# Kernel tuning notes

Measured on AMD Instinct MI355X. Metric: run time of the kernel, lower is better.

Reference implementation:

```python
import math
import jax, jax.numpy as jnp
import numpy as np

T = 4096
D_MODEL = 1024
NUM_HEADS = 16
HEAD_DIM = D_MODEL // NUM_HEADS


def setup_inputs() -> dict:
    key = jax.random.key(0)
    k_x, k_wqkv, k_wproj = jax.random.split(key, 3)
    # match eqx.nn.Linear init scale: U(-1/sqrt(in), 1/sqrt(in)); randn*small works too,
    # but keep magnitudes reasonable so softmax isn't saturated.
    s_in = 1.0 / math.sqrt(D_MODEL)
    x = jax.random.normal(k_x, (T, D_MODEL), dtype=jnp.float32)
    W_qkv = jax.random.normal(k_wqkv, (3 * D_MODEL, D_MODEL), dtype=jnp.float32) * s_in
    b_qkv = jnp.zeros((3 * D_MODEL,), dtype=jnp.float32)
    W_proj = jax.random.normal(k_wproj, (D_MODEL, D_MODEL), dtype=jnp.float32) * s_in
    b_proj = jnp.zeros((D_MODEL,), dtype=jnp.float32)
    return {"x": x, "W_qkv": W_qkv, "b_qkv": b_qkv, "W_proj": W_proj, "b_proj": b_proj}


def reference(x, W_qkv, b_qkv, W_proj, b_proj):
    T_, C = x.shape  # (seq, d_model)
    H, hd = NUM_HEADS, HEAD_DIM
    # c_attn: eqx Linear computes W @ x + b per token -> x @ W.T + b
    qkv = x @ W_qkv.T + b_qkv  # (T, 3C)
    q, k, v = jnp.split(qkv, 3, axis=1)
    # (T, C) -> (H, T, hd)
    q = q.reshape(T_, H, hd).swapaxes(0, 1)
    k = k.reshape(T_, H, hd).swapaxes(0, 1)
    v = v.reshape(T_, H, hd).swapaxes(0, 1)
    scores = jnp.einsum("htd,hsd->hts", q, k) / math.sqrt(hd)  # (H, T, T)
    causal = jnp.tril(jnp.ones((T_, T_), dtype=bool))
    scores = jnp.where(causal, scores, -jnp.inf)
    attn = jax.nn.softmax(scores, axis=-1)
    y = jnp.einsum("hts,hsd->htd", attn, v)  # (H, T, hd)
    y = y.swapaxes(0, 1).reshape(T_, C)
    y = y @ W_proj.T + b_proj
    return y
```

## Files before the change

### kernel.cpp

```cpp
#include <hip/hip_runtime.h>
#include <math.h>
#include <string.h>

#define T_SEQ 4096
#define DM 1024
#define NH 16
#define HD 64

typedef short s8v __attribute__((ext_vector_type(8)));
typedef float f4v __attribute__((ext_vector_type(4)));

__device__ inline unsigned short f2bf(float f) {
    unsigned u; memcpy(&u, &f, 4);
    u = u + 0x7fffu + ((u >> 16) & 1u);
    return (unsigned short)(u >> 16);
}

__device__ inline float exp2fn(float x) {
#if __has_builtin(__builtin_amdgcn_exp2f)
    return __builtin_amdgcn_exp2f(x);
#else
    return exp2f(x);
#endif
}

__device__ inline void gld_lds16(const void* g, void* l) {
    __builtin_amdgcn_global_load_lds(
        (const __attribute__((address_space(1))) void*)g,
        (__attribute__((address_space(3))) void*)l, 16, 0, 0);
}

__global__ __launch_bounds__(256)
void cvt_bf16(const float* __restrict__ in, unsigned short* __restrict__ out, int n8) {
    int i = blockIdx.x * 256 + threadIdx.x;
    if (i >= n8) return;
    const float4* p = (const float4*)(in + (size_t)i * 8);
    float4 a = p[0], b = p[1];
    unsigned short o[8] = {f2bf(a.x), f2bf(a.y), f2bf(a.z), f2bf(a.w),
                           f2bf(b.x), f2bf(b.y), f2bf(b.z), f2bf(b.w)};
    uint4 pk; memcpy(&pk, o, 16);
    *(uint4*)(out + (size_t)i * 8) = pk;
}

template<int MODE>
__global__ __launch_bounds__(256)
void gemm_bt_mfma(const unsigned short* __restrict__ A, const unsigned short* __restrict__ B,
                  const float* __restrict__ bias, void* __restrict__ Cout,
                  unsigned short* __restrict__ vT,
                  int M, int N, int K) {
    __shared__ __align__(16) short As[512 * 8];
    __shared__ __align__(16) short Bs[512 * 8];
    const int tid = threadIdx.x;
    const int w = tid >> 6, lane = tid & 63;
    const int wr = w >> 1, wc = w & 1;
    const int m0 = blockIdx.y * 128, n0 = blockIdx.x * 128;

    const unsigned short* src = (w < 2) ? A : B;
    const int rbase = ((w < 2) ? m0 : n0) + (w & 1) * 64;
    const unsigned short* gsrc = src + (size_t)(rbase + (lane & 15)) * K + ((lane >> 4) * 8);
    short* ldst = ((w < 2) ? As : Bs) + ((w & 1) * 4) * 512;

    f4v acc[4][4];
    #pragma unroll
    for (int i = 0; i < 4; ++i)
        #pragma unroll
        for (int j = 0; j < 4; ++j) acc[i][j] = (f4v){0.f, 0.f, 0.f, 0.f};

    for (int k0 = 0; k0 < K; k0 += 32) {
        __syncthreads();
        #pragma unroll
        for (int i = 0; i < 4; ++i)
            gld_lds16(gsrc + (size_t)(i * 16) * K + k0, ldst + i * 512);
        __syncthreads();

        s8v af[4], bf[4];
        #pragma unroll
        for (int i = 0; i < 4; ++i) af[i] = *(const s8v*)&As[((wr * 4 + i) * 64 + lane) * 8];
        #pragma unroll
        for (int j = 0; j < 4; ++j) bf[j] = *(const s8v*)&Bs[((wc * 4 + j) * 64 + lane) * 8];
        #pragma unroll
        for (int i = 0; i < 4; ++i)
            #pragma unroll
            for (int j = 0; j < 4; ++j)
                acc[i][j] = __builtin_amdgcn_mfma_f32_16x16x32_bf16(af[i], bf[j], acc[i][j], 0, 0, 0);
    }

    const int l15 = lane & 15, quad = lane >> 4;
    float bj[4];
    #pragma unroll
    for (int j = 0; j < 4; ++j) bj[j] = bias[n0 + wc * 64 + j * 16 + l15];

    if (MODE == 2 && n0 >= 2 * DM) {
        #pragma unroll
        for (int i = 0; i < 4; ++i) {
            int tb = m0 + wr * 64 + i * 16 + quad * 4;
            #pragma unroll
            for (int j = 0; j < 4; ++j) {
                int dg = n0 - 2 * DM + wc * 64 + j * 16 + l15;
                unsigned short o[4];
                #pragma unroll
                for (int rg = 0; rg < 4; ++rg) o[rg] = f2bf(acc[i][j][rg] + bj[j]);
                unsigned long long pk; memcpy(&pk, o, 8);
                *(unsigned long long*)&vT[(size_t)dg * T_SEQ + tb] = pk;
            }
        }
    } else {
        #pragma unroll
        for (int i = 0; i < 4; ++i) {
            #pragma unroll
            for (int rg = 0; rg < 4; ++rg) {
                int row = m0 + wr * 64 + i * 16 + quad * 4 + rg;
                #pragma unroll
                for (int j = 0; j < 4; ++j) {
                    int col = n0 + wc * 64 + j * 16 + l15;
                    float v = acc[i][j][rg] + bj[j];
                    if (MODE == 0) ((float*)Cout)[(size_t)row * N + col] = v;
                    else           ((unsigned short*)Cout)[(size_t)row * N + col] = f2bf(v);
                }
            }
        }
    }
}

__global__ __launch_bounds__(256, 2)
void attn_mfma2(const unsigned short* __restrict__ qkv,
                const unsigned short* __restrict__ vT,
                unsigned short* __restrict__ y) {
    const int b = blockIdx.x;
    const int h = b & 15, a = b >> 4;
    const int tid = threadIdx.x;
    const int w = tid >> 6, lane = tid & 63;
    const int quad = lane >> 4, l15 = lane & 15;
    const int cq = h * HD, hv = h * HD;
    const size_t rs = 3 * DM;
    const float C2 = 0.1803368851f;

    __shared__ short KB[2][4096];
    __shared__ short VTs[2][4096];
    __shared__ short QB[4096];
    __shared__ short PB[4][1024];

    for (int ph = 0; ph < 2; ++ph) {
        const int qt = ph ? (63 - a) : a;
        const int q0 = qt * 64;

        __syncthreads();
        #pragma unroll
        for (int rr = 0; rr < 2; ++rr) {
            int ch = rr * 256 + tid;
            int blk = ch >> 7, hf = (ch >> 6) & 1, ln = ch & 63;
            const unsigned short* gq = qkv + (size_t)(q0 + blk * 16 + (ln & 15)) * rs
                                     + cq + hf * 32 + ((ln >> 4) << 3);
            gld_lds16(gq, &QB[(ch & ~63) * 8]);
            const unsigned short* gk = qkv + (size_t)(blk * 16 + (ln & 15)) * rs
                                     + DM + cq + hf * 32 + ((ln >> 4) << 3);
            gld_lds16(gk, &KB[0][(ch & ~63) * 8]);
            const unsigned short* gv = vT + (size_t)(hv + blk * 16 + (ln & 15)) * T_SEQ
                                     + hf * 32 + ((ln >> 4) << 3);
            gld_lds16(gv, &VTs[0][(ch & ~63) * 8]);
        }
        __syncthreads();

        s8v qf0 = *(const s8v*)&QB[((w * 2 + 0) * 64 + lane) * 8];
        s8v qf1 = *(const s8v*)&QB[((w * 2 + 1) * 64 + lane) * 8];

        f4v O[4];
        #pragma unroll
        for (int ob = 0; ob < 4; ++ob) O[ob] = (f4v){0.f, 0.f, 0.f, 0.f};
        float mr = -3.0e38f, lr = 0.f;

        for (int kt = 0; kt <= qt; ++kt) {
            const int p = kt & 1;
            if (kt < qt) {
                const int k1 = (kt + 1) * 64;
                #pragma unroll
                for (int rr = 0; rr < 2; ++rr) {
                    int ch = rr * 256 + tid;
                    int blk = ch >> 7, hf = (ch >> 6) & 1, ln = ch & 63;
                    const unsigned short* gk = qkv + (size_t)(k1 + blk * 16 + (ln & 15)) * rs
                                             + DM + cq + hf * 32 + ((ln >> 4) << 3);
                    gld_lds16(gk, &KB[p ^ 1][(ch & ~63) * 8]);
                    const unsigned short* gv = vT + (size_t)(hv + blk * 16 + (ln & 15)) * T_SEQ
                                             + k1 + hf * 32 + ((ln >> 4) << 3);
                    gld_lds16(gv, &VTs[p ^ 1][(ch & ~63) * 8]);
                }
            }

            f4v st[4];
            #pragma unroll
            for (int kb = 0; kb < 4; ++kb) {
                s8v k0f = *(const s8v*)&KB[p][((kb * 2 + 0) * 64 + lane) * 8];
                s8v k1f = *(const s8v*)&KB[p][((kb * 2 + 1) * 64 + lane) * 8];
                f4v c = (f4v){0.f, 0.f, 0.f, 0.f};
                c = __builtin_amdgcn_mfma_f32_16x16x32_bf16(k0f, qf0, c, 0, 0, 0);
                c = __builtin_amdgcn_mfma_f32_16x16x32_bf16(k1f, qf1, c, 0, 0, 0);
                st[kb] = c;
            }

            float sv[4][4];
            #pragma unroll
            for (int kb = 0; kb < 4; ++kb)
                #pragma unroll
                for (int rg = 0; rg < 4; ++rg) sv[kb][rg] = st[kb][rg];
            if (kt == qt) {
                #pragma unroll
                for (int kb = 0; kb < 4; ++kb) {
                    #pragma unroll
                    for (int rg = 0; rg < 4; ++rg)
                        if (kb * 16 + quad * 4 + rg > w * 16 + l15) sv[kb][rg] = -3.0e38f;
                }
            }

            float mx = sv[0][0];
            #pragma unroll
            for (int kb = 0; kb < 4; ++kb)
                #pragma unroll
                for (int rg = 0; rg < 4; ++rg) mx = fmaxf(mx, sv[kb][rg]);
            mx = fmaxf(mx, __shfl_xor(mx, 16));
            mx = fmaxf(mx, __shfl_xor(mx, 32));
            float mn = fmaxf(mr, mx);
            float alpha = exp2fn((mr - mn) * C2);
            float mc = mn * C2;
            float ps = 0.f;
            #pragma unroll
            for (int kb = 0; kb < 4; ++kb)
                #pragma unroll
                for (int rg = 0; rg < 4; ++rg) {
                    float t = exp2fn(fmaf(sv[kb][rg], C2, -mc));
                    sv[kb][rg] = t;
                    ps += t;
                }
            ps += __shfl_xor(ps, 16);
            ps += __shfl_xor(ps, 32);
            lr = lr * alpha + ps;
            mr = mn;
            #pragma unroll
            for (int ob = 0; ob < 4; ++ob)
                #pragma unroll
                for (int rg = 0; rg < 4; ++rg) O[ob][rg] *= alpha;

            short* pw = PB[w];
            #pragma unroll
            for (int kb = 0; kb < 4; ++kb) {
                unsigned u0 = __float_as_uint(sv[kb][0]) + 0x8000u;
                unsigned u1 = __float_as_uint(sv[kb][1]) + 0x8000u;
                unsigned u2 = __float_as_uint(sv[kb][2]) + 0x8000u;
                unsigned u3 = __float_as_uint(sv[kb][3]) + 0x8000u;
                int2 v;
                v.x = (int)__builtin_amdgcn_perm(u1, u0, 0x07060302);
                v.y = (int)__builtin_amdgcn_perm(u3, u2, 0x07060302);
                int c = (kb >> 1) * 64 + ((kb & 1) * 2 + (quad >> 1)) * 16 + l15;
                c ^= ((c >> 3) & 7);
                *(int2*)&pw[c * 8 + (quad & 1) * 4] = v;
            }
            asm volatile("s_waitcnt lgkmcnt(0)" ::: "memory");
            int c0 = lane ^ ((lane >> 3) & 7);
            s8v pf0 = *(const s8v*)&pw[c0 * 8];
            s8v pf1 = *(const s8v*)&pw[(64 + c0) * 8];

            #pragma unroll
            for (int ob = 0; ob < 4; ++ob) {
                s8v v0f = *(const s8v*)&VTs[p][((ob * 2 + 0) * 64 + lane) * 8];
                s8v v1f = *(const s8v*)&VTs[p][((ob * 2 + 1) * 64 + lane) * 8];
                O[ob] = __builtin_amdgcn_mfma_f32_16x16x32_bf16(v0f, pf0, O[ob], 0, 0, 0);
                O[ob] = __builtin_amdgcn_mfma_f32_16x16x32_bf16(v1f, pf1, O[ob], 0, 0, 0);
            }
            __syncthreads();
        }

        float linv = 1.f / lr;
        size_t ybase = (size_t)(q0 + w * 16 + l15) * DM + cq;
        #pragma unroll
        for (int ob = 0; ob < 4; ++ob) {
            unsigned short o[4];
            #pragma unroll
            for (int rg = 0; rg < 4; ++rg) o[rg] = f2bf(O[ob][rg] * linv);
            unsigned long long pk; memcpy(&pk, o, 8);
            *(unsigned long long*)&y[ybase + ob * 16 + quad * 4] = pk;
        }
    }
}

extern "C" void kernel_launch(void* const* d_in, const int* in_sizes, int n_in,
                              void* d_out, int out_size, void* d_ws, size_t ws_size,
                              hipStream_t stream) {
    const float* x     = (const float*)d_in[0];
    const float* Wqkv  = (const float*)d_in[1];
    const float* bqkv  = (const float*)d_in[2];
    const float* Wproj = (const float*)d_in[3];
    const float* bproj = (const float*)d_in[4];
    float* out = (float*)d_out;

    char* ws = (char*)d_ws;
    unsigned short* qkvb  = (unsigned short*)(ws);
    unsigned short* yattb = (unsigned short*)(ws + (24u << 20));
    unsigned short* xb    = (unsigned short*)(ws + (32u << 20));
    unsigned short* wqkvb = (unsigned short*)(ws + (40u << 20));
    unsigned short* wprjb = (unsigned short*)(ws + (46u << 20));
    unsigned short* vTb   = (unsigned short*)(ws + (48u << 20));

    dim3 blk(256);
    {
        int n8;
        n8 = T_SEQ * DM / 8;
        cvt_bf16<<<dim3((n8 + 255) / 256), blk, 0, stream>>>(x, xb, n8);
        n8 = 3 * DM * DM / 8;
        cvt_bf16<<<dim3((n8 + 255) / 256), blk, 0, stream>>>(Wqkv, wqkvb, n8);
        n8 = DM * DM / 8;
        cvt_bf16<<<dim3((n8 + 255) / 256), blk, 0, stream>>>(Wproj, wprjb, n8);
    }
    gemm_bt_mfma<2><<<dim3(3 * DM / 128, T_SEQ / 128), blk, 0, stream>>>(
        xb, wqkvb, bqkv, qkvb, vTb, T_SEQ, 3 * DM, DM);
    attn_mfma2<<<dim3(NH * 32), blk, 0, stream>>>(qkvb, vTb, yattb);
    gemm_bt_mfma<0><<<dim3(DM / 128, T_SEQ / 128), blk, 0, stream>>>(
        yattb, wprjb, bproj, out, nullptr, T_SEQ, DM, DM);
}
```

Before: 242.2 us.

## Use 128-row query tiles in attention, fuse conversions, narrow proj GEMM tile

The attention kernel now gives each block one 128-row query tile split into two 64-row groups that share every staged K/V tile. This halves K/V loads per query and removes the two-phase loop. The three fp32-to-bf16 conversions become a single launch, cutting launch overhead. The output projection GEMM uses a 64-wide N tile so it launches more blocks, at the cost of less reuse per block and idle staging warps.

```diff
diff --git a/kernel.cpp b/kernel.cpp
--- a/kernel.cpp
+++ b/kernel.cpp
@@ -31,72 +31,83 @@
 }
 
 __global__ __launch_bounds__(256)
-void cvt_bf16(const float* __restrict__ in, unsigned short* __restrict__ out, int n8) {
+void cvt3(const float* __restrict__ i0, unsigned short* __restrict__ o0, int n0,
+          const float* __restrict__ i1, unsigned short* __restrict__ o1, int n1,
+          const float* __restrict__ i2, unsigned short* __restrict__ o2, int n2) {
     int i = blockIdx.x * 256 + threadIdx.x;
-    if (i >= n8) return;
-    const float4* p = (const float4*)(in + (size_t)i * 8);
+    const float* in; unsigned short* out; int j;
+    if (i < n0)           { in = i0; out = o0; j = i; }
+    else if (i < n0 + n1) { in = i1; out = o1; j = i - n0; }
+    else if (i < n0 + n1 + n2) { in = i2; out = o2; j = i - n0 - n1; }
+    else return;
+    const float4* p = (const float4*)(in + (size_t)j * 8);
     float4 a = p[0], b = p[1];
     unsigned short o[8] = {f2bf(a.x), f2bf(a.y), f2bf(a.z), f2bf(a.w),
                            f2bf(b.x), f2bf(b.y), f2bf(b.z), f2bf(b.w)};
     uint4 pk; memcpy(&pk, o, 16);
-    *(uint4*)(out + (size_t)i * 8) = pk;
-}
-
-template<int MODE>
+    *(uint4*)(out + (size_t)j * 8) = pk;
+}
+
+template<int MODE, int TN>
 __global__ __launch_bounds__(256)
 void gemm_bt_mfma(const unsigned short* __restrict__ A, const unsigned short* __restrict__ B,
                   const float* __restrict__ bias, void* __restrict__ Cout,
                   unsigned short* __restrict__ vT,
                   int M, int N, int K) {
-    __shared__ __align__(16) short As[512 * 8];
-    __shared__ __align__(16) short Bs[512 * 8];
+    constexpr int NF = TN / 32;
+    __shared__ __align__(16) short As[4096];
+    __shared__ __align__(16) short Bs[TN * 32];
     const int tid = threadIdx.x;
     const int w = tid >> 6, lane = tid & 63;
     const int wr = w >> 1, wc = w & 1;
-    const int m0 = blockIdx.y * 128, n0 = blockIdx.x * 128;
-
-    const unsigned short* src = (w < 2) ? A : B;
-    const int rbase = ((w < 2) ? m0 : n0) + (w & 1) * 64;
+    const int m0 = blockIdx.y * 128, n0 = blockIdx.x * TN;
+
+    const bool doA = (w < 2);
+    const bool doStage = doA || ((w & 1) * 64 < TN);
+    const unsigned short* src = doA ? A : B;
+    const int rbase = (doA ? m0 : n0) + (w & 1) * 64;
     const unsigned short* gsrc = src + (size_t)(rbase + (lane & 15)) * K + ((lane >> 4) * 8);
-    short* ldst = ((w < 2) ? As : Bs) + ((w & 1) * 4) * 512;
-
-    f4v acc[4][4];
+    short* ldst = (doA ? As : Bs) + ((w & 1) * 4) * 512;
+
+    f4v acc[4][NF];
     #pragma unroll
     for (int i = 0; i < 4; ++i)
         #pragma unroll
-        for (int j = 0; j < 4; ++j) acc[i][j] = (f4v){0.f, 0.f, 0.f, 0.f};
+        for (int j = 0; j < NF; ++j) acc[i][j] = (f4v){0.f, 0.f, 0.f, 0.f};
 
     for (int k0 = 0; k0 < K; k0 += 32) {
         __syncthreads();
+        if (doStage) {
+            #pragma unroll
+            for (int i = 0; i < 4; ++i)
+                gld_lds16(gsrc + (size_t)(i * 16) * K + k0, ldst + i * 512);
+        }
+        __syncthreads();
+
+        s8v af[4], bf[NF];
+        #pragma unroll
+        for (int i = 0; i < 4; ++i) af[i] = *(const s8v*)&As[((wr * 4 + i) * 64 + lane) * 8];
+        #pragma unroll
+        for (int j = 0; j < NF; ++j) bf[j] = *(const s8v*)&Bs[((wc * NF + j) * 64 + lane) * 8];
         #pragma unroll
         for (int i = 0; i < 4; ++i)
-            gld_lds16(gsrc + (size_t)(i * 16) * K + k0, ldst + i * 512);
-        __syncthreads();
-
-        s8v af[4], bf[4];
-        #pragma unroll
-        for (int i = 0; i < 4; ++i) af[i] = *(const s8v*)&As[((wr * 4 + i) * 64 + lane) * 8];
-        #pragma unroll
-        for (int j = 0; j < 4; ++j) bf[j] = *(const s8v*)&Bs[((wc * 4 + j) * 64 + lane) * 8];
-        #pragma unroll
-        for (int i = 0; i < 4; ++i)
-            #pragma unroll
-            for (int j = 0; j < 4; ++j)
+            #pragma unroll
+            for (int j = 0; j < NF; ++j)
                 acc[i][j] = __builtin_amdgcn_mfma_f32_16x16x32_bf16(af[i], bf[j], acc[i][j], 0, 0, 0);
     }
 
     const int l15 = lane & 15, quad = lane >> 4;
-    float bj[4];
-    #pragma unroll
-    for (int j = 0; j < 4; ++j) bj[j] = bias[n0 + wc * 64 + j * 16 + l15];
+    float bj[NF];
+    #pragma unroll
+    for (int j = 0; j < NF; ++j) bj[j] = bias[n0 + wc * (TN / 2) + j * 16 + l15];
 
     if (MODE == 2 && n0 >= 2 * DM) {
         #pragma unroll
         for (int i = 0; i < 4; ++i) {
             int tb = m0 + wr * 64 + i * 16 + quad * 4;
             #pragma unroll
-            for (int j = 0; j < 4; ++j) {
-                int dg = n0 - 2 * DM + wc * 64 + j * 16 + l15;
+            for (int j = 0; j < NF; ++j) {
+                int dg = n0 - 2 * DM + wc * (TN / 2) + j * 16 + l15;
                 unsigned short o[4];
                 #pragma unroll
                 for (int rg = 0; rg < 4; ++rg) o[rg] = f2bf(acc[i][j][rg] + bj[j]);
@@ -111,8 +122,8 @@
             for (int rg = 0; rg < 4; ++rg) {
                 int row = m0 + wr * 64 + i * 16 + quad * 4 + rg;
                 #pragma unroll
-                for (int j = 0; j < 4; ++j) {
-                    int col = n0 + wc * 64 + j * 16 + l15;
+                for (int j = 0; j < NF; ++j) {
+                    int col = n0 + wc * (TN / 2) + j * 16 + l15;
                     float v = acc[i][j][rg] + bj[j];
                     if (MODE == 0) ((float*)Cout)[(size_t)row * N + col] = v;
                     else           ((unsigned short*)Cout)[(size_t)row * N + col] = f2bf(v);
@@ -122,154 +133,184 @@
     }
 }
 
+__device__ __forceinline__ void online_step(f4v* st, bool diag, int qloc, int quad, int l15,
+                                            float& mr, float& lr, f4v* O, short* pw) {
+    const float C2 = 0.1803368851f;
+    float sv[4][4];
+    #pragma unroll
+    for (int kb = 0; kb < 4; ++kb)
+        #pragma unroll
+        for (int rg = 0; rg < 4; ++rg) sv[kb][rg] = st[kb][rg];
+    if (diag) {
+        #pragma unroll
+        for (int kb = 0; kb < 4; ++kb)
+            #pragma unroll
+            for (int rg = 0; rg < 4; ++rg)
+                if (kb * 16 + quad * 4 + rg > qloc) sv[kb][rg] = -3.0e38f;
+    }
+    float mx = sv[0][0];
+    #pragma unroll
+    for (int kb = 0; kb < 4; ++kb)
+        #pragma unroll
+        for (int rg = 0; rg < 4; ++rg) mx = fmaxf(mx, sv[kb][rg]);
+    mx = fmaxf(mx, __shfl_xor(mx, 16));
+    mx = fmaxf(mx, __shfl_xor(mx, 32));
+    float mn = fmaxf(mr, mx);
+    float alpha = exp2fn((mr - mn) * C2);
+    float mc = mn * C2;
+    float ps = 0.f;
+    #pragma unroll
+    for (int kb = 0; kb < 4; ++kb)
+        #pragma unroll
+        for (int rg = 0; rg < 4; ++rg) {
+            float t = exp2fn(fmaf(sv[kb][rg], C2, -mc));
+            sv[kb][rg] = t;
+            ps += t;
+        }
+    ps += __shfl_xor(ps, 16);
+    ps += __shfl_xor(ps, 32);
+    lr = lr * alpha + ps;
+    mr = mn;
+    #pragma unroll
+    for (int ob = 0; ob < 4; ++ob)
+        #pragma unroll
+        for (int rg = 0; rg < 4; ++rg) O[ob][rg] *= alpha;
+    #pragma unroll
+    for (int kb = 0; kb < 4; ++kb) {
+        unsigned u0 = __float_as_uint(sv[kb][0]) + 0x8000u;
+        unsigned u1 = __float_as_uint(sv[kb][1]) + 0x8000u;
+        unsigned u2 = __float_as_uint(sv[kb][2]) + 0x8000u;
+        unsigned u3 = __float_as_uint(sv[kb][3]) + 0x8000u;
+        int2 v;
+        v.x = (int)__builtin_amdgcn_perm(u1, u0, 0x07060302);
+        v.y = (int)__builtin_amdgcn_perm(u3, u2, 0x07060302);
+        int c = (kb >> 1) * 64 + ((kb & 1) * 2 + (quad >> 1)) * 16 + l15;
+        c ^= ((c >> 3) & 7);
+        *(int2*)&pw[c * 8 + (quad & 1) * 4] = v;
+    }
+}
+
 __global__ __launch_bounds__(256, 2)
-void attn_mfma2(const unsigned short* __restrict__ qkv,
+void attn_mfma3(const unsigned short* __restrict__ qkv,
                 const unsigned short* __restrict__ vT,
                 unsigned short* __restrict__ y) {
     const int b = blockIdx.x;
-    const int h = b & 15, a = b >> 4;
+    const int half = b >> 8, i = b & 255;
+    const int h = i & 15, t8 = i >> 4;
+    const int qt = half ? (31 - 2 * t8) : (2 * t8);
     const int tid = threadIdx.x;
     const int w = tid >> 6, lane = tid & 63;
     const int quad = lane >> 4, l15 = lane & 15;
     const int cq = h * HD, hv = h * HD;
     const size_t rs = 3 * DM;
-    const float C2 = 0.1803368851f;
+    const int q0 = qt * 128;
+    const int lastk = 2 * qt + 1;
 
     __shared__ short KB[2][4096];
     __shared__ short VTs[2][4096];
-    __shared__ short QB[4096];
-    __shared__ short PB[4][1024];
-
-    for (int ph = 0; ph < 2; ++ph) {
-        const int qt = ph ? (63 - a) : a;
-        const int q0 = qt * 64;
-
+    __shared__ short QB[8192];
+    __shared__ short PB[8][1024];
+
+    #pragma unroll
+    for (int rr = 0; rr < 4; ++rr) {
+        int ch = rr * 256 + tid;
+        int qg = ch >> 7, hf = (ch >> 6) & 1, ln = ch & 63;
+        gld_lds16(qkv + (size_t)(q0 + qg * 16 + (ln & 15)) * rs + cq + hf * 32 + ((ln >> 4) << 3),
+                  &QB[(ch & ~63) * 8]);
+    }
+    #pragma unroll
+    for (int rr = 0; rr < 2; ++rr) {
+        int ch = rr * 256 + tid;
+        int blk = ch >> 7, hf = (ch >> 6) & 1, ln = ch & 63;
+        gld_lds16(qkv + (size_t)(blk * 16 + (ln & 15)) * rs + DM + cq + hf * 32 + ((ln >> 4) << 3),
+                  &KB[0][(ch & ~63) * 8]);
+        gld_lds16(vT + (size_t)(hv + blk * 16 + (ln & 15)) * T_SEQ + hf * 32 + ((ln >> 4) << 3),
+                  &VTs[0][(ch & ~63) * 8]);
+    }
+    __syncthreads();
+
+    s8v qf[2][2];
+    #pragma unroll
+    for (int g = 0; g < 2; ++g)
+        #pragma unroll
+        for (int hf = 0; hf < 2; ++hf)
+            qf[g][hf] = *(const s8v*)&QB[((((g * 4 + w) * 2 + hf) * 64) + lane) * 8];
+
+    f4v O0[4], O1[4];
+    #pragma unroll
+    for (int ob = 0; ob < 4; ++ob) {
+        O0[ob] = (f4v){0.f, 0.f, 0.f, 0.f};
+        O1[ob] = (f4v){0.f, 0.f, 0.f, 0.f};
+    }
+    float mr0 = -3.0e38f, lr0 = 0.f, mr1 = -3.0e38f, lr1 = 0.f;
+
+    for (int kt = 0; kt <= lastk; ++kt) {
+        const int p = kt & 1;
+        const bool g0a = (kt < lastk);
+        if (kt < lastk) {
+            const int k1 = (kt + 1) * 64;
+            #pragma unroll
+            for (int rr = 0; rr < 2; ++rr) {
+                int ch = rr * 256 + tid;
+                int blk = ch >> 7, hf = (ch >> 6) & 1, ln = ch & 63;
+                gld_lds16(qkv + (size_t)(k1 + blk * 16 + (ln & 15)) * rs + DM + cq
+                              + hf * 32 + ((ln >> 4) << 3),
+                          &KB[p ^ 1][(ch & ~63) * 8]);
+                gld_lds16(vT + (size_t)(hv + blk * 16 + (ln & 15)) * T_SEQ + k1
+                              + hf * 32 + ((ln >> 4) << 3),
+                          &VTs[p ^ 1][(ch & ~63) * 8]);
+            }
+        }
+
+        f4v st0[4], st1[4];
+        #pragma unroll
+        for (int kb = 0; kb < 4; ++kb) {
+            s8v k0f = *(const s8v*)&KB[p][((kb * 2 + 0) * 64 + lane) * 8];
+            s8v k1f = *(const s8v*)&KB[p][((kb * 2 + 1) * 64 + lane) * 8];
+            f4v c1 = (f4v){0.f, 0.f, 0.f, 0.f};
+            c1 = __builtin_amdgcn_mfma_f32_16x16x32_bf16(k0f, qf[1][0], c1, 0, 0, 0);
+            c1 = __builtin_amdgcn_mfma_f32_16x16x32_bf16(k1f, qf[1][1], c1, 0, 0, 0);
+            st1[kb] = c1;
+            if (g0a) {
+                f4v c0 = (f4v){0.f, 0.f, 0.f, 0.f};
+                c0 = __builtin_amdgcn_mfma_f32_16x16x32_bf16(k0f, qf[0][0], c0, 0, 0, 0);
+                c0 = __builtin_amdgcn_mfma_f32_16x16x32_bf16(k1f, qf[0][1], c0, 0, 0, 0);
+                st0[kb] = c0;
+            }
+        }
+
+        if (g0a) online_step(st0, kt == lastk - 1, w * 16 + l15, quad, l15, mr0, lr0, O0, PB[w * 2 + 0]);
+        online_step(st1, kt == lastk, w * 16 + l15, quad, l15, mr1, lr1, O1, PB[w * 2 + 1]);
+
+        asm volatile("s_waitcnt lgkmcnt(0)" ::: "memory");
+        int c0i = lane ^ ((lane >> 3) & 7);
+        s8v pf10 = *(const s8v*)&PB[w * 2 + 1][c0i * 8];
+        s8v pf11 = *(const s8v*)&PB[w * 2 + 1][(64 + c0i) * 8];
+        s8v pf00, pf01;
+        if (g0a) {
+            pf00 = *(const s8v*)&PB[w * 2 + 0][c0i * 8];
+            pf01 = *(const s8v*)&PB[w * 2 + 0][(64 + c0i) * 8];
+        }
+
+        #pragma unroll
+        for (int ob = 0; ob < 4; ++ob) {
+            s8v v0f = *(const s8v*)&VTs[p][((ob * 2 + 0) * 64 + lane) * 8];
+            s8v v1f = *(const s8v*)&VTs[p][((ob * 2 + 1) * 64 + lane) * 8];
+            O1[ob] = __builtin_amdgcn_mfma_f32_16x16x32_bf16(v0f, pf10, O1[ob], 0, 0, 0);
+            O1[ob] = __builtin_amdgcn_mfma_f32_16x16x32_bf16(v1f, pf11, O1[ob], 0, 0, 0);
+            if (g0a) {
+                O0[ob] = __builtin_amdgcn_mfma_f32_16x16x32_bf16(v0f, pf00, O0[ob], 0, 0, 0);
+                O0[ob] = __builtin_amdgcn_mfma_f32_16x16x32_bf16(v1f, pf01, O0[ob], 0, 0, 0);
+            }
+        }
         __syncthreads();
-        #pragma unroll
-        for (int rr = 0; rr < 2; ++rr) {
-            int ch = rr * 256 + tid;
-            int blk = ch >> 7, hf = (ch >> 6) & 1, ln = ch & 63;
-            const unsigned short* gq = qkv + (size_t)(q0 + blk * 16 + (ln & 15)) * rs
-                                     + cq + hf * 32 + ((ln >> 4) << 3);
-            gld_lds16(gq, &QB[(ch & ~63) * 8]);
-            const unsigned short* gk = qkv + (size_t)(blk * 16 + (ln & 15)) * rs
-                                     + DM + cq + hf * 32 + ((ln >> 4) << 3);
-            gld_lds16(gk, &KB[0][(ch & ~63) * 8]);
-            const unsigned short* gv = vT + (size_t)(hv + blk * 16 + (ln & 15)) * T_SEQ
-                                     + hf * 32 + ((ln >> 4) << 3);
-            gld_lds16(gv, &VTs[0][(ch & ~63) * 8]);
-        }
-        __syncthreads();
-
-        s8v qf0 = *(const s8v*)&QB[((w * 2 + 0) * 64 + lane) * 8];
-        s8v qf1 = *(const s8v*)&QB[((w * 2 + 1) * 64 + lane) * 8];
-
-        f4v O[4];
-        #pragma unroll
-        for (int ob = 0; ob < 4; ++ob) O[ob] = (f4v){0.f, 0.f, 0.f, 0.f};
-        float mr = -3.0e38f, lr = 0.f;
-
-        for (int kt = 0; kt <= qt; ++kt) {
-            const int p = kt & 1;
-            if (kt < qt) {
-                const int k1 = (kt + 1) * 64;
-                #pragma unroll
-                for (int rr = 0; rr < 2; ++rr) {
-                    int ch = rr * 256 + tid;
-                    int blk = ch >> 7, hf = (ch >> 6) & 1, ln = ch & 63;
-                    const unsigned short* gk = qkv + (size_t)(k1 + blk * 16 + (ln & 15)) * rs
-                                             + DM + cq + hf * 32 + ((ln >> 4) << 3);
-                    gld_lds16(gk, &KB[p ^ 1][(ch & ~63) * 8]);
-                    const unsigned short* gv = vT + (size_t)(hv + blk * 16 + (ln & 15)) * T_SEQ
-                                             + k1 + hf * 32 + ((ln >> 4) << 3);
-                    gld_lds16(gv, &VTs[p ^ 1][(ch & ~63) * 8]);
-                }
-            }
-
-            f4v st[4];
-            #pragma unroll
-            for (int kb = 0; kb < 4; ++kb) {
-                s8v k0f = *(const s8v*)&KB[p][((kb * 2 + 0) * 64 + lane) * 8];
-                s8v k1f = *(const s8v*)&KB[p][((kb * 2 + 1) * 64 + lane) * 8];
-                f4v c = (f4v){0.f, 0.f, 0.f, 0.f};
-                c = __builtin_amdgcn_mfma_f32_16x16x32_bf16(k0f, qf0, c, 0, 0, 0);
-                c = __builtin_amdgcn_mfma_f32_16x16x32_bf16(k1f, qf1, c, 0, 0, 0);
-                st[kb] = c;
-            }
-
-            float sv[4][4];
-            #pragma unroll
-            for (int kb = 0; kb < 4; ++kb)
-                #pragma unroll
-                for (int rg = 0; rg < 4; ++rg) sv[kb][rg] = st[kb][rg];
-            if (kt == qt) {
-                #pragma unroll
-                for (int kb = 0; kb < 4; ++kb) {
-                    #pragma unroll
-                    for (int rg = 0; rg < 4; ++rg)
-                        if (kb * 16 + quad * 4 + rg > w * 16 + l15) sv[kb][rg] = -3.0e38f;
-                }
-            }
-
-            float mx = sv[0][0];
-            #pragma unroll
-            for (int kb = 0; kb < 4; ++kb)
-                #pragma unroll
-                for (int rg = 0; rg < 4; ++rg) mx = fmaxf(mx, sv[kb][rg]);
-            mx = fmaxf(mx, __shfl_xor(mx, 16));
-            mx = fmaxf(mx, __shfl_xor(mx, 32));
-            float mn = fmaxf(mr, mx);
-            float alpha = exp2fn((mr - mn) * C2);
-            float mc = mn * C2;
-            float ps = 0.f;
-            #pragma unroll
-            for (int kb = 0; kb < 4; ++kb)
-                #pragma unroll
-                for (int rg = 0; rg < 4; ++rg) {
-                    float t = exp2fn(fmaf(sv[kb][rg], C2, -mc));
-                    sv[kb][rg] = t;
-                    ps += t;
-                }
-            ps += __shfl_xor(ps, 16);
-            ps += __shfl_xor(ps, 32);
-            lr = lr * alpha + ps;
-            mr = mn;
-            #pragma unroll
-            for (int ob = 0; ob < 4; ++ob)
-                #pragma unroll
-                for (int rg = 0; rg < 4; ++rg) O[ob][rg] *= alpha;
-
-            short* pw = PB[w];
-            #pragma unroll
-            for (int kb = 0; kb < 4; ++kb) {
-                unsigned u0 = __float_as_uint(sv[kb][0]) + 0x8000u;
-                unsigned u1 = __float_as_uint(sv[kb][1]) + 0x8000u;
-                unsigned u2 = __float_as_uint(sv[kb][2]) + 0x8000u;
-                unsigned u3 = __float_as_uint(sv[kb][3]) + 0x8000u;
-                int2 v;
-                v.x = (int)__builtin_amdgcn_perm(u1, u0, 0x07060302);
-                v.y = (int)__builtin_amdgcn_perm(u3, u2, 0x07060302);
-                int c = (kb >> 1) * 64 + ((kb & 1) * 2 + (quad >> 1)) * 16 + l15;
-                c ^= ((c >> 3) & 7);
-                *(int2*)&pw[c * 8 + (quad & 1) * 4] = v;
-            }
-            asm volatile("s_waitcnt lgkmcnt(0)" ::: "memory");
-            int c0 = lane ^ ((lane >> 3) & 7);
-            s8v pf0 = *(const s8v*)&pw[c0 * 8];
-            s8v pf1 = *(const s8v*)&pw[(64 + c0) * 8];
-
-            #pragma unroll
-            for (int ob = 0; ob < 4; ++ob) {
-                s8v v0f = *(const s8v*)&VTs[p][((ob * 2 + 0) * 64 + lane) * 8];
-                s8v v1f = *(const s8v*)&VTs[p][((ob * 2 + 1) * 64 + lane) * 8];
-                O[ob] = __builtin_amdgcn_mfma_f32_16x16x32_bf16(v0f, pf0, O[ob], 0, 0, 0);
-                O[ob] = __builtin_amdgcn_mfma_f32_16x16x32_bf16(v1f, pf1, O[ob], 0, 0, 0);
-            }
-            __syncthreads();
-        }
-
-        float linv = 1.f / lr;
-        size_t ybase = (size_t)(q0 + w * 16 + l15) * DM + cq;
+    }
+
+    #pragma unroll
+    for (int g = 0; g < 2; ++g) {
+        float linv = 1.f / (g ? lr1 : lr0);
+        const f4v* O = g ? O1 : O0;
+        size_t ybase = (size_t)(q0 + g * 64 + w * 16 + l15) * DM + cq;
         #pragma unroll
         for (int ob = 0; ob < 4; ++ob) {
             unsigned short o[4];
@@ -301,17 +342,13 @@
 
     dim3 blk(256);
     {
-        int n8;
-        n8 = T_SEQ * DM / 8;
-        cvt_bf16<<<dim3((n8 + 255) / 256), blk, 0, stream>>>(x, xb, n8);
-        n8 = 3 * DM * DM / 8;
-        cvt_bf16<<<dim3((n8 + 255) / 256), blk, 0, stream>>>(Wqkv, wqkvb, n8);
-        n8 = DM * DM / 8;
-        cvt_bf16<<<dim3((n8 + 255) / 256), blk, 0, stream>>>(Wproj, wprjb, n8);
-    }
-    gemm_bt_mfma<2><<<dim3(3 * DM / 128, T_SEQ / 128), blk, 0, stream>>>(
+        int n0 = T_SEQ * DM / 8, n1 = 3 * DM * DM / 8, n2 = DM * DM / 8;
+        cvt3<<<dim3((n0 + n1 + n2 + 255) / 256), blk, 0, stream>>>(
+            x, xb, n0, Wqkv, wqkvb, n1, Wproj, wprjb, n2);
+    }
+    gemm_bt_mfma<2, 128><<<dim3(3 * DM / 128, T_SEQ / 128), blk, 0, stream>>>(
         xb, wqkvb, bqkv, qkvb, vTb, T_SEQ, 3 * DM, DM);
-    attn_mfma2<<<dim3(NH * 32), blk, 0, stream>>>(qkvb, vTb, yattb);
-    gemm_bt_mfma<0><<<dim3(DM / 128, T_SEQ / 128), blk, 0, stream>>>(
+    attn_mfma3<<<dim3(NH * T_SEQ / 128), blk, 0, stream>>>(qkvb, vTb, yattb);
+    gemm_bt_mfma<0, 64><<<dim3(DM / 64, T_SEQ / 128), blk, 0, stream>>>(
         yattb, wprjb, bproj, out, nullptr, T_SEQ, DM, DM);
 }
```

After: 276.2 us. 14.0% more time.
